# Kernel optimization log

Hardware: AMD Instinct MI355X
Metric: run time of the kernel (lower is better)

Reference implementation:

```python
import jax, jax.numpy as jnp
import numpy as np
from jax import lax

H = 128  # LSTM hidden size (hardcoded in module)

def setup_inputs() -> dict:
    key = jax.random.key(0)
    ks = jax.random.split(key, 10)
    B, S, D = 256, 512, 80
    T = 3
    s_in = 1.0 / np.sqrt(D)
    s_h = 1.0 / np.sqrt(H)
    return {
        "x": jax.random.normal(ks[0], (B, S, D), dtype=jnp.float32),
        "W_in": jax.random.uniform(ks[1], (256, D), jnp.float32, -s_in, s_in),
        "b_in": jax.random.uniform(ks[2], (256,), jnp.float32, -s_in, s_in),
        "W_ih": jax.random.uniform(ks[3], (4 * H, 256), jnp.float32, -s_h, s_h),
        "b_ih": jax.random.uniform(ks[4], (4 * H,), jnp.float32, -s_h, s_h),
        "W_hh": jax.random.uniform(ks[5], (4 * H, H), jnp.float32, -s_h, s_h),
        "b_hh": jax.random.uniform(ks[6], (4 * H,), jnp.float32, -s_h, s_h),
        "w_time": jax.random.uniform(ks[7], (T,), jnp.float32, -1.0 / np.sqrt(T), 1.0 / np.sqrt(T)),
        "W_br": jax.random.uniform(ks[8], (4, H), jnp.float32, -s_h, s_h),
        "b_br": jax.random.uniform(ks[9], (4,), jnp.float32, -s_h, s_h),
        "batch_size": B,
        "time_steps": T,
    }


def reference(x, W_in, b_in, W_ih, b_ih, W_hh, b_hh, w_time, W_br, b_br, batch_size, time_steps):
    # input projection (dropout is identity in eval mode)
    xl = jnp.einsum('bsd,ed->bse', x, W_in) + b_in  # [B,S,256]
    B, S, _ = xl.shape
    T = time_steps

    def step(carry, inp):
        h, c, h_st, c_st = carry
        xt, i = inp  # xt: [B,256], i: step index
        gates = xt @ W_ih.T + b_ih + h @ W_hh.T + b_hh  # [B,4H]
        ig, fg, gg, og = jnp.split(gates, 4, axis=-1)
        c_new = jax.nn.sigmoid(fg) * c + jax.nn.sigmoid(ig) * jnp.tanh(gg)
        h_new = jax.nn.sigmoid(og) * jnp.tanh(c_new)
        slot = i % T
        oh = jax.nn.one_hot(slot, T, dtype=h_new.dtype)  # [T]
        h_st = h_st * (1.0 - oh) + h_new[:, :, None] * oh  # [B,H,T]
        c_st = c_st * (1.0 - oh) + c_new[:, :, None] * oh
        pool = (slot == T - 1)
        ph = jnp.einsum('bht,t->bh', h_st, w_time)
        pc = jnp.einsum('bht,t->bh', c_st, w_time)
        h_out = jnp.where(pool, ph, h_new)
        c_out = jnp.where(pool, pc, c_new)
        h_st = jnp.where(pool, jnp.zeros_like(h_st), h_st)
        c_st = jnp.where(pool, jnp.zeros_like(c_st), c_st)
        return (h_out, c_out, h_st, c_st), h_out

    init = (jnp.zeros((B, H), xl.dtype), jnp.zeros((B, H), xl.dtype),
            jnp.zeros((B, H, T), xl.dtype), jnp.zeros((B, H, T), xl.dtype))
    _, outs = lax.scan(step, init, (jnp.swapaxes(xl, 0, 1), jnp.arange(S)))
    out = jnp.swapaxes(outs, 0, 1)  # [B,S,H]
    logits = jnp.einsum('bsh,oh->bso', out, W_br) + b_br  # [B,S,4]
    return jax.nn.log_softmax(logits, axis=2)
```

## Files before the change

kernel.cpp:

```cpp
#include <hip/hip_runtime.h>
#include <hip/hip_fp16.h>

#define BB 256
#define SS 512
#define DD 80
#define HH 128
#define GG 512

typedef _Float16 h2_t __attribute__((ext_vector_type(2)));
typedef _Float16 half8 __attribute__((ext_vector_type(8)));
typedef float f32x4 __attribute__((ext_vector_type(4)));

union U32H2 { unsigned int u; h2_t h; unsigned short us[2]; };

static __device__ __forceinline__ h2_t u2h(unsigned int u) { U32H2 x; x.u = u; return x.h; }

static __device__ __forceinline__ unsigned int pk2(float a, float b) {
  unsigned int lo = (unsigned int)__half_as_ushort(__float2half(a));
  unsigned int hi = (unsigned int)__half_as_ushort(__float2half(b));
  return (hi << 16) | lo;
}

static __device__ __forceinline__ float fdot2(unsigned int a, unsigned int b, float c) {
#if __has_builtin(__builtin_amdgcn_fdot2)
  return __builtin_amdgcn_fdot2(u2h(a), u2h(b), c, false);
#else
  U32H2 ua, ub; ua.u = a; ub.u = b;
  return c + (float)ua.h[0] * (float)ub.h[0] + (float)ua.h[1] * (float)ub.h[1];
#endif
}

static __device__ __forceinline__ float fsig(float x) {
  return __fdividef(1.f, 1.f + __expf(-x));
}

__global__ __launch_bounds__(128) void prep_kernel(
    const float* __restrict__ W_in, const float* __restrict__ b_in,
    const float* __restrict__ W_ih, const float* __restrict__ b_ih,
    const float* __restrict__ W_hh, const float* __restrict__ b_hh,
    unsigned short* __restrict__ wc16, unsigned short* __restrict__ whh16,
    float* __restrict__ biasc)
{
  const int g = blockIdx.x;
  const int t = threadIdx.x;
  const float* wih = W_ih + g * 256;
  if (t < DD) {
    float s = 0.f;
    for (int e = 0; e < 256; ++e) s += wih[e] * W_in[e * DD + t];
    wc16[g * DD + t] = __half_as_ushort(__float2half(s));
  }
  whh16[g * HH + t] = __half_as_ushort(__float2half(W_hh[g * HH + t]));
  if (t == 0) {
    float s = 0.f;
    for (int e = 0; e < 256; ++e) s += wih[e] * b_in[e];
    biasc[g] = s + b_ih[g] + b_hh[g];
  }
}

__global__ __launch_bounds__(256) void gemm_kernel(
    const float* __restrict__ x,
    const unsigned int* __restrict__ wc,
    uint4* __restrict__ gx)
{
  __shared__ unsigned int Al[64 * 52];
  __shared__ unsigned int Bl[128 * 52];
  const int t  = threadIdx.x;
  const int mt = blockIdx.x;
  const int g0 = blockIdx.y * 128;

  {
    const float4* xr = (const float4*)(x + (size_t)mt * 64 * DD);
    #pragma unroll
    for (int i = 0; i < 5; ++i) {
      int f = t + i * 256;
      int row = f / 20, c4 = f % 20;
      float4 v = xr[row * 20 + c4];
      Al[row * 52 + c4 * 2]     = pk2(v.x, v.y);
      Al[row * 52 + c4 * 2 + 1] = pk2(v.z, v.w);
    }
    #pragma unroll
    for (int i = 0; i < 3; ++i) {
      int f = t + i * 256;
      int row = f / 12, c = f % 12;
      Al[row * 52 + 40 + c] = 0u;
    }
  }
  {
    #pragma unroll
    for (int i = 0; i < 5; ++i) {
      int f = t + i * 256;
      int row = f / 10, c4 = f % 10;
      uint4 v = *(const uint4*)(wc + (size_t)(g0 + row) * 40 + c4 * 4);
      *(uint4*)&Bl[row * 52 + c4 * 4] = v;
    }
    #pragma unroll
    for (int i = 0; i < 6; ++i) {
      int f = t + i * 256;
      int row = f / 12, c = f % 12;
      Bl[row * 52 + 40 + c] = 0u;
    }
  }
  __syncthreads();

  const int w = t >> 6, lane = t & 63;
  const int m = lane & 15, q = lane >> 4;

  half8 af[3];
  #pragma unroll
  for (int kk = 0; kk < 3; ++kk)
    af[kk] = *(const half8*)((const char*)Al + (size_t)(w * 16 + m) * 208 + kk * 64 + q * 16);

  #pragma unroll
  for (int j = 0; j < 8; ++j) {
    f32x4 acc = {0.f, 0.f, 0.f, 0.f};
    #pragma unroll
    for (int kk = 0; kk < 3; ++kk) {
      half8 bf = *(const half8*)((const char*)Bl + (size_t)(j * 16 + m) * 208 + kk * 64 + q * 16);
      acc = __builtin_amdgcn_mfma_f32_16x16x32_f16(af[kk], bf, acc, 0, 0, 0);
    }
    unsigned int lo  = pk2(acc[0], acc[1]);
    unsigned int hi  = pk2(acc[2], acc[3]);
    unsigned int plo = (unsigned int)__shfl_down((int)lo, 16);
    unsigned int phi = (unsigned int)__shfl_down((int)hi, 16);
    if ((q & 1) == 0) {
      const int gl  = g0 + j * 16 + m;
      const int col = ((gl & 127) << 2) | (gl >> 7);
      uint4 o; o.x = lo; o.y = hi; o.z = plo; o.w = phi;
      gx[((size_t)mt * 8 + w * 2 + (q >> 1)) * 512 + (size_t)col] = o;
    }
  }
}

__global__ __attribute__((amdgpu_waves_per_eu(2, 2))) __launch_bounds__(512)
void scan_kernel(
    const uint4* __restrict__ gx,
    const uint4* __restrict__ whh,
    const float* __restrict__ biasc,
    const float* __restrict__ wtime,
    __half* __restrict__ hout)
{
  __shared__ unsigned int hbuf[2][64];
  const int b    = blockIdx.x;
  const int t    = threadIdx.x;
  const int lane = t & 63;
  const int q    = t & 3;
  const int hi2  = t >> 2;
  const int g    = q * 128 + hi2;

  unsigned int w[64];
  {
    const uint4* wr = whh + (size_t)g * 16;
    #pragma unroll
    for (int i = 0; i < 16; ++i) {
      uint4 v = wr[i];
      w[4*i] = v.x; w[4*i+1] = v.y; w[4*i+2] = v.z; w[4*i+3] = v.w;
    }
  }
  const float bias = biasc[g];
  const float wt0 = wtime[0], wt1 = wtime[1], wt2 = wtime[2];
  if (t < 64) { hbuf[0][t] = 0u; hbuf[1][t] = 0u; }
  float c = 0.f, hst0 = 0.f, hst1 = 0.f, cst0 = 0.f, cst1 = 0.f;
  int slot = 0, s = 0;
  const uint4* gxp = gx + (size_t)b * 64 * 512 + t;
  __syncthreads();

  uint4 gv = gxp[0];
  for (int sb = 0; sb < 64; ++sb) {
    uint4 gn = gv;
    if (sb < 63) gn = gxp[(size_t)(sb + 1) * 512];
    unsigned int ga[4] = {gv.x, gv.y, gv.z, gv.w};
    #pragma unroll
    for (int i = 0; i < 8; ++i) {
      const int par = s & 1;
      const unsigned int hreg = hbuf[par][lane];
      U32H2 gu; gu.u = ga[i >> 1];
      const float gxi = (float)gu.h[i & 1];
      float d0 = bias + gxi, d1 = 0.f, d2 = 0.f, d3 = 0.f;
      #pragma unroll
      for (int p = 0; p < 64; p += 4) {
        int h0 = __builtin_amdgcn_readlane((int)hreg, p);
        int h1 = __builtin_amdgcn_readlane((int)hreg, p + 1);
        int h2 = __builtin_amdgcn_readlane((int)hreg, p + 2);
        int h3 = __builtin_amdgcn_readlane((int)hreg, p + 3);
        d0 = fdot2(w[p],     (unsigned int)h0, d0);
        d1 = fdot2(w[p + 1], (unsigned int)h1, d1);
        d2 = fdot2(w[p + 2], (unsigned int)h2, d2);
        d3 = fdot2(w[p + 3], (unsigned int)h3, d3);
      }
      const float d = (d0 + d1) + (d2 + d3);
      const float din = (q == 2) ? d + d : d;
      const float sv  = fsig(din);
      const float a   = (q == 2) ? 2.f * sv - 1.f : sv;
      const float v1 = __shfl_xor(a, 1);
      const float v2 = __shfl_xor(a, 2);
      const float v3 = __shfl_xor(a, 3);
      const int b0 = q & 1, b1 = q >> 1;
      const float iv = b1 ? (b0 ? v3 : v2) : (b0 ? v1 : a);
      const float fv = b1 ? (b0 ? v2 : v3) : (b0 ? a  : v1);
      const float gg = b1 ? (b0 ? v1 : a ) : (b0 ? v3 : v2);
      const float ov = b1 ? (b0 ? a  : v1) : (b0 ? v2 : v3);
      c = fv * c + iv * gg;
      const float tc = 2.f * fsig(c + c) - 1.f;
      const float hn = ov * tc;
      float hcur;
      if (slot == 2) {
        hcur = hst0 * wt0 + hst1 * wt1 + hn * wt2;
        c    = cst0 * wt0 + cst1 * wt1 + c  * wt2;
        slot = 0;
      } else {
        hcur = hn;
        if (slot == 0) { hst0 = hn; cst0 = c; }
        else           { hst1 = hn; cst1 = c; }
        ++slot;
      }
      if (q == 0) {
        const __half hh2 = __float2half(hcur);
        ((__half*)hbuf[par ^ 1])[hi2] = hh2;
        hout[((size_t)b * SS + s) * HH + hi2] = hh2;
      }
      ++s;
      __syncthreads();
    }
    gv = gn;
  }
}

__global__ __launch_bounds__(256) void out_kernel(
    const uint4* __restrict__ hout,
    const float* __restrict__ Wbr, const float* __restrict__ bbr,
    float4* __restrict__ out)
{
  __shared__ unsigned int wb[4][64];
  __shared__ float bbs[4];
  const int t = threadIdx.x;
  {
    const int o = t >> 6, p = t & 63;
    wb[o][p] = pk2(Wbr[o * HH + 2 * p], Wbr[o * HH + 2 * p + 1]);
  }
  if (t < 4) bbs[t] = bbr[t];
  __syncthreads();

  const size_t row = (size_t)blockIdx.x * 256 + t;
  const uint4* hr = hout + row * 16;
  float a0 = bbs[0], a1 = bbs[1], a2 = bbs[2], a3 = bbs[3];
  #pragma unroll
  for (int qq = 0; qq < 16; ++qq) {
    uint4 hv = hr[qq];
    unsigned int hd[4] = {hv.x, hv.y, hv.z, hv.w};
    #pragma unroll
    for (int d = 0; d < 4; ++d) {
      const int p = qq * 4 + d;
      a0 = fdot2(hd[d], wb[0][p], a0);
      a1 = fdot2(hd[d], wb[1][p], a1);
      a2 = fdot2(hd[d], wb[2][p], a2);
      a3 = fdot2(hd[d], wb[3][p], a3);
    }
  }
  const float m = fmaxf(fmaxf(a0, a1), fmaxf(a2, a3));
  const float e0 = __expf(a0 - m), e1 = __expf(a1 - m), e2 = __expf(a2 - m), e3 = __expf(a3 - m);
  const float lse = m + __logf(e0 + e1 + e2 + e3);
  out[row] = make_float4(a0 - lse, a1 - lse, a2 - lse, a3 - lse);
}

extern "C" void kernel_launch(void* const* d_in, const int* in_sizes, int n_in,
                              void* d_out, int out_size, void* d_ws, size_t ws_size,
                              hipStream_t stream) {
  const float* x     = (const float*)d_in[0];
  const float* W_in  = (const float*)d_in[1];
  const float* b_in  = (const float*)d_in[2];
  const float* W_ih  = (const float*)d_in[3];
  const float* b_ih  = (const float*)d_in[4];
  const float* W_hh  = (const float*)d_in[5];
  const float* b_hh  = (const float*)d_in[6];
  const float* wtime = (const float*)d_in[7];
  const float* W_br  = (const float*)d_in[8];
  const float* b_br  = (const float*)d_in[9];
  (void)in_sizes; (void)n_in; (void)out_size; (void)ws_size;

  char* ws = (char*)d_ws;
  unsigned short* wc16  = (unsigned short*)(ws + 0);
  unsigned short* whh16 = (unsigned short*)(ws + 81920);
  float*          biasc = (float*)(ws + 212992);
  __half*         hout  = (__half*)(ws + 215040);
  uint4*          gx    = (uint4*)(ws + 33769472);

  prep_kernel<<<512, 128, 0, stream>>>(W_in, b_in, W_ih, b_ih, W_hh, b_hh,
                                       wc16, whh16, biasc);
  gemm_kernel<<<dim3(2048, 4), 256, 0, stream>>>(x, (const unsigned int*)wc16, gx);
  scan_kernel<<<256, 512, 0, stream>>>(gx, (const uint4*)whh16, biasc, wtime, hout);
  out_kernel<<<512, 256, 0, stream>>>((const uint4*)hout, W_br, b_br, (float4*)d_out);
}
```

Before: 684.8 us.

## Compute recurrent h·W_hh with MFMA instead of per-lane fdot2 readlane loop

Replaces the per-thread 64-step fdot2 dot product, which broadcast h via readlane, with MFMA 16x16x32 f16 matrix ops. Each wave holds a 64-row slice of W_hh as A fragments, reads h from LDS as B fragments, and writes gate pre-activations to a shared buffer that each thread then reads for its gate. This adds an extra block-wide barrier and LDS round trip per timestep, and the inner timestep loop is no longer unrolled. The B operand broadcasts the same h vector across all columns, so most of each MFMA's work is redundant.

```diff
diff --git a/kernel.cpp b/kernel.cpp
--- a/kernel.cpp
+++ b/kernel.cpp
@@ -12,6 +12,7 @@
 typedef float f32x4 __attribute__((ext_vector_type(4)));
 
 union U32H2 { unsigned int u; h2_t h; unsigned short us[2]; };
+union U4H8 { uint4 u; half8 h; };
 
 static __device__ __forceinline__ h2_t u2h(unsigned int u) { U32H2 x; x.u = u; return x.h; }
 
@@ -140,22 +141,31 @@
     __half* __restrict__ hout)
 {
   __shared__ unsigned int hbuf[2][64];
+  __shared__ float gbuf[512];
   const int b    = blockIdx.x;
   const int t    = threadIdx.x;
-  const int lane = t & 63;
+  const int L    = t & 63;
+  const int wv   = t >> 6;
   const int q    = t & 3;
   const int hi2  = t >> 2;
   const int g    = q * 128 + hi2;
 
-  unsigned int w[64];
+  half8 af[16];
   {
-    const uint4* wr = whh + (size_t)g * 16;
-    #pragma unroll
-    for (int i = 0; i < 16; ++i) {
-      uint4 v = wr[i];
-      w[4*i] = v.x; w[4*i+1] = v.y; w[4*i+2] = v.z; w[4*i+3] = v.w;
-    }
-  }
+    const int gr = wv * 64 + (L & 15);
+    #pragma unroll
+    for (int tt = 0; tt < 4; ++tt) {
+      #pragma unroll
+      for (int kk = 0; kk < 4; ++kk) {
+        U4H8 u;
+        u.u = whh[(size_t)(gr + tt * 16) * 16 + kk * 4 + (L >> 4)];
+        af[tt * 4 + kk] = u.h;
+      }
+    }
+  }
+  #pragma unroll
+  for (int i = 0; i < 16; ++i) asm volatile("" : "+v"(af[i]));
+
   const float bias = biasc[g];
   const float wt0 = wtime[0], wt1 = wtime[1], wt2 = wtime[2];
   if (t < 64) { hbuf[0][t] = 0u; hbuf[1][t] = 0u; }
@@ -169,25 +179,27 @@
     uint4 gn = gv;
     if (sb < 63) gn = gxp[(size_t)(sb + 1) * 512];
     unsigned int ga[4] = {gv.x, gv.y, gv.z, gv.w};
-    #pragma unroll
+    #pragma unroll 1
     for (int i = 0; i < 8; ++i) {
       const int par = s & 1;
-      const unsigned int hreg = hbuf[par][lane];
+      half8 bf[4];
+      #pragma unroll
+      for (int kk = 0; kk < 4; ++kk)
+        bf[kk] = *(const half8*)((const char*)hbuf[par] + kk * 64 + (L >> 4) * 16);
+      #pragma unroll
+      for (int tt = 0; tt < 4; ++tt) {
+        f32x4 acc = {0.f, 0.f, 0.f, 0.f};
+        #pragma unroll
+        for (int kk = 0; kk < 4; ++kk)
+          acc = __builtin_amdgcn_mfma_f32_16x16x32_f16(af[tt * 4 + kk], bf[kk], acc, 0, 0, 0);
+        if ((L & 15) == 0)
+          *(f32x4*)&gbuf[wv * 64 + tt * 16 + (L >> 4) * 4] = acc;
+      }
+      __syncthreads();
+
       U32H2 gu; gu.u = ga[i >> 1];
       const float gxi = (float)gu.h[i & 1];
-      float d0 = bias + gxi, d1 = 0.f, d2 = 0.f, d3 = 0.f;
-      #pragma unroll
-      for (int p = 0; p < 64; p += 4) {
-        int h0 = __builtin_amdgcn_readlane((int)hreg, p);
-        int h1 = __builtin_amdgcn_readlane((int)hreg, p + 1);
-        int h2 = __builtin_amdgcn_readlane((int)hreg, p + 2);
-        int h3 = __builtin_amdgcn_readlane((int)hreg, p + 3);
-        d0 = fdot2(w[p],     (unsigned int)h0, d0);
-        d1 = fdot2(w[p + 1], (unsigned int)h1, d1);
-        d2 = fdot2(w[p + 2], (unsigned int)h2, d2);
-        d3 = fdot2(w[p + 3], (unsigned int)h3, d3);
-      }
-      const float d = (d0 + d1) + (d2 + d3);
+      const float d = gbuf[g] + bias + gxi;
       const float din = (q == 2) ? d + d : d;
       const float sv  = fsig(din);
       const float a   = (q == 2) ? 2.f * sv - 1.f : sv;
```

Result: faster. 635.4 us (-7.2%).
